# Kernel tuning notes

Hardware: AMD Instinct MI355X
Metric: run time of the kernel (lower is better)

## Reference

```python
import jax, jax.numpy as jnp
import numpy as np

D_MODEL = 1024
HEADS = 16
DK = D_MODEL // HEADS
B, S = 2, 2048


def setup_inputs() -> dict:
    key = jax.random.key(0)
    ks = jax.random.split(key, 9)
    s = 0.02
    return {
        "Q": jax.random.normal(ks[0], (B, S, D_MODEL), jnp.float32),
        "K": jax.random.normal(ks[1], (B, S, D_MODEL), jnp.float32),
        "V": jax.random.normal(ks[2], (B, S, D_MODEL), jnp.float32),
        "mask": jnp.ones((B, 1, S), jnp.int32),
        "Wq": jax.random.normal(ks[3], (D_MODEL, D_MODEL), jnp.float32) * s,
        "Wk": jax.random.normal(ks[4], (D_MODEL, D_MODEL), jnp.float32) * s,
        "Wv": jax.random.normal(ks[5], (D_MODEL, D_MODEL), jnp.float32) * s,
        "Wo": jax.random.normal(ks[6], (D_MODEL, D_MODEL), jnp.float32) * s,
        "ln_gamma": jnp.ones((D_MODEL,), jnp.float32),
        "ln_beta": jnp.zeros((D_MODEL,), jnp.float32),
    }


def _layer_norm(x, gamma, beta, eps=1e-5):
    mu = jnp.mean(x, axis=-1, keepdims=True)
    var = jnp.mean(jnp.square(x - mu), axis=-1, keepdims=True)
    return (x - mu) * jax.lax.rsqrt(var + eps) * gamma + beta


def reference(Q, K, V, mask, Wq, Wk, Wv, Wo, ln_gamma, ln_beta):
    # torch Linear(no bias): y = x @ W.T
    def split_heads(x):  # [B,S,D] -> [B,H,S,dk]
        return x.reshape(B, -1, HEADS, DK).transpose(0, 2, 1, 3)

    q = split_heads(Q @ Wq.T)
    k = split_heads(K @ Wk.T)
    v = split_heads(V @ Wv.T)

    # scores: [B,H,Sq,Sk]
    scores = jnp.einsum("bhqd,bhkd->bhqk", q, k) / np.sqrt(DK).astype(np.float32)
    m = mask[:, None, :, :]  # [B,1,1,S] broadcast over heads and queries
    scores = jnp.where(m == 0, -jnp.inf, scores)
    attn = jax.nn.softmax(scores, axis=-1)  # dropout is identity in eval
    out = jnp.einsum("bhqk,bhkd->bhqd", attn, v)
    out = out.transpose(0, 2, 1, 3).reshape(B, -1, D_MODEL)
    out = out @ Wo.T
    return _layer_norm(out + Q, ln_gamma, ln_beta)
```

## Files before the change

kernel.cpp:

```cpp
#include <hip/hip_runtime.h>
#include <hip/hip_bf16.h>
#include <stdint.h>

#define NB 2
#define NS 2048
#define ND 1024
#define NH 16
#define NDK 64
#define NM (NB*NS)

using bf16x8 = __attribute__((ext_vector_type(8))) short;
using f32x4  = __attribute__((ext_vector_type(4))) float;
using f32x16 = __attribute__((ext_vector_type(16))) float;
using u32x4  = __attribute__((ext_vector_type(4))) unsigned;

__device__ __forceinline__ unsigned short f2bf(float f){
  unsigned u = __float_as_uint(f);
  u += 0x7fffu + ((u>>16)&1u);
  return (unsigned short)(u>>16);
}

__device__ __forceinline__ void gload_lds16(const void* g, void* l){
  __builtin_amdgcn_global_load_lds((const __attribute__((address_space(1))) void*)g,
                                   (__attribute__((address_space(3))) void*)l, 16, 0, 0);
}

__device__ __forceinline__ float fexp2(float x){
#if __has_builtin(__builtin_amdgcn_exp2f)
  return __builtin_amdgcn_exp2f(x);
#else
  return __expf(x * 0.69314718056f);
#endif
}

__device__ __forceinline__ unsigned cvtpk_bf16(float lo, float hi){
  unsigned r;
  asm("v_cvt_pk_bf16_f32 %0, %1, %2" : "=v"(r) : "v"(lo), "v"(hi));
  return r;
}

__device__ __forceinline__ void swap32(unsigned &a, unsigned &b){
#if __has_builtin(__builtin_amdgcn_permlane32_swap)
  auto rr = __builtin_amdgcn_permlane32_swap((int)a, (int)b, false, false);
  a = (unsigned)rr[0]; b = (unsigned)rr[1];
#else
  const bool lo = (threadIdx.x & 32) == 0;
  unsigned sa = (unsigned)__shfl_xor((int)a, 32, 64);
  unsigned sb = (unsigned)__shfl_xor((int)b, 32, 64);
  unsigned na = lo ? a : sb;
  unsigned nb = lo ? sa : b;
  a = na; b = nb;
#endif
}

__device__ __forceinline__ f32x16 mfma32(bf16x8 a, bf16x8 b, f32x16 c){
  return __builtin_amdgcn_mfma_f32_32x32x16_bf16(a, b, c, 0, 0, 0);
}

__global__ __launch_bounds__(256) void prep_k(const float* __restrict__ Q, const float* __restrict__ K,
                                              const float* __restrict__ V, const float* __restrict__ Wq,
                                              const float* __restrict__ Wk, const float* __restrict__ Wv,
                                              const float* __restrict__ Wo,
                                              unsigned short* __restrict__ Xbf,
                                              unsigned short* __restrict__ Wbf){
  const int bid = blockIdx.x;
  const float* src; unsigned short* dst; int i;
  if (bid < 12288){
    const int which = bid >> 12;
    src = (which==0) ? Q : (which==1) ? K : V;
    dst = Xbf + ((size_t)which << 22);
    i = (bid & 4095)*256 + threadIdx.x;
  } else {
    const int which = (bid - 12288) >> 10;
    src = (which==0) ? Wq : (which==1) ? Wk : (which==2) ? Wv : Wo;
    dst = Wbf + ((size_t)which << 20);
    i = ((bid - 12288) & 1023)*256 + threadIdx.x;
  }
  float4 v = ((const float4*)src)[i];
  ushort4 o;
  o.x = f2bf(v.x); o.y = f2bf(v.y); o.z = f2bf(v.z); o.w = f2bf(v.w);
  ((ushort4*)dst)[i] = o;
}

__global__ __launch_bounds__(256) void gemm_qkv(const short* __restrict__ Xbf, const short* __restrict__ Wbf,
                                                unsigned short* __restrict__ qh, unsigned short* __restrict__ kh,
                                                unsigned short* __restrict__ vT){
  __shared__ short lsA[2][4096];
  __shared__ short lsB[2][4096];
  const int tid = threadIdx.x;
  const int hw = blockIdx.x;
  const int logical = (hw & 7)*96 + (hw >> 3);
  const int z = logical >> 8, rem = logical & 255;
  const int my = rem >> 3, nx = rem & 7;
  const short* A = Xbf + (size_t)z*NM*ND;
  const short* W = Wbf + (size_t)z*ND*ND;
  unsigned short* out = (z==0) ? qh : (z==1) ? kh : vT;
  const int mode = (z==2) ? 1 : 0;
  const int m0 = my*128, n0 = nx*128;

  const short* gA = A + (size_t)m0*1024;
  const short* gB = W + (size_t)n0*1024;
  const int srow = tid>>2;
  const int scol = ((tid&3)*8) ^ (((srow>>1)&3)<<3);
  const int w = tid>>6, lane = tid&63, lr = lane&15, lk = lane>>4;
  const int wm = w>>1, wn = w&1;

  f32x4 acc[4][4];
  #pragma unroll
  for (int i=0;i<4;++i)
    #pragma unroll
    for (int j=0;j<4;++j) acc[i][j] = (f32x4){0.f,0.f,0.f,0.f};

  #pragma unroll
  for (int r=0;r<2;++r){
    gload_lds16(gA + (size_t)(r*64+srow)*1024 + scol, &lsA[0][(r*256+tid)*8]);
    gload_lds16(gB + (size_t)(r*64+srow)*1024 + scol, &lsB[0][(r*256+tid)*8]);
  }
  int cur = 0;
  for (int ks=0; ks<32; ++ks){
    __syncthreads();
    if (ks+1 < 32){
      const int k0 = (ks+1)*32;
      #pragma unroll
      for (int r=0;r<2;++r){
        gload_lds16(gA + (size_t)(r*64+srow)*1024 + k0 + scol, &lsA[cur^1][(r*256+tid)*8]);
        gload_lds16(gB + (size_t)(r*64+srow)*1024 + k0 + scol, &lsB[cur^1][(r*256+tid)*8]);
      }
    }
    bf16x8 af[4], bfr[4];
    const char* Ab = (const char*)&lsA[cur][0];
    const char* Bb = (const char*)&lsB[cur][0];
    #pragma unroll
    for (int i=0;i<4;++i){
      const int ra = wm*64 + i*16 + lr;
      const int rb = wn*64 + i*16 + lr;
      af[i]  = *(const bf16x8*)(Ab + ra*64 + ((lk*16) ^ (((ra>>1)&3)<<4)));
      bfr[i] = *(const bf16x8*)(Bb + rb*64 + ((lk*16) ^ (((rb>>1)&3)<<4)));
    }
    #pragma unroll
    for (int i=0;i<4;++i)
      #pragma unroll
      for (int j=0;j<4;++j)
        acc[i][j] = __builtin_amdgcn_mfma_f32_16x16x32_bf16(af[i], bfr[j], acc[i][j], 0,0,0);
    cur ^= 1;
  }
  #pragma unroll
  for (int i=0;i<4;++i)
    #pragma unroll
    for (int j=0;j<4;++j)
      #pragma unroll
      for (int r=0;r<4;++r){
        const int m = m0 + wm*64 + i*16 + lk*4 + r;
        const int n = n0 + wn*64 + j*16 + lr;
        const float v = acc[i][j][r];
        const int b = m>>11, s = m&2047, h = n>>6, dk = n&63;
        size_t addr;
        if (mode == 0) addr = (((size_t)(b*NH+h))*NS + s)*NDK + dk;
        else           addr = (((size_t)(b*NH+h))*NDK + dk)*NS + s;
        out[addr] = f2bf(v);
      }
}

__global__ __launch_bounds__(256) void gemm_out(const short* __restrict__ Attn, const short* __restrict__ Wo,
                                                const float* __restrict__ Qin, float* __restrict__ proj){
  __shared__ short lsA[2][4096];
  __shared__ short lsB[2][4096];
  const int tid = threadIdx.x;
  const int hw = blockIdx.x;
  const int logical = (hw & 7)*32 + (hw >> 3);
  const int my = logical >> 3, nx = logical & 7;
  const int m0 = my*128, n0 = nx*128;
  const short* gA = Attn + (size_t)m0*1024;
  const short* gB = Wo + (size_t)n0*1024;
  const int srow = tid>>2;
  const int scol = ((tid&3)*8) ^ (((srow>>1)&3)<<3);
  const int w = tid>>6, lane = tid&63, lr = lane&15, lk = lane>>4;
  const int wm = w>>1, wn = w&1;

  f32x4 acc[4][4];
  #pragma unroll
  for (int i=0;i<4;++i)
    #pragma unroll
    for (int j=0;j<4;++j) acc[i][j] = (f32x4){0.f,0.f,0.f,0.f};

  #pragma unroll
  for (int r=0;r<2;++r){
    gload_lds16(gA + (size_t)(r*64+srow)*1024 + scol, &lsA[0][(r*256+tid)*8]);
    gload_lds16(gB + (size_t)(r*64+srow)*1024 + scol, &lsB[0][(r*256+tid)*8]);
  }
  int cur = 0;
  for (int ks=0; ks<32; ++ks){
    __syncthreads();
    if (ks+1 < 32){
      const int k0 = (ks+1)*32;
      #pragma unroll
      for (int r=0;r<2;++r){
        gload_lds16(gA + (size_t)(r*64+srow)*1024 + k0 + scol, &lsA[cur^1][(r*256+tid)*8]);
        gload_lds16(gB + (size_t)(r*64+srow)*1024 + k0 + scol, &lsB[cur^1][(r*256+tid)*8]);
      }
    }
    bf16x8 af[4], bfr[4];
    const char* Ab = (const char*)&lsA[cur][0];
    const char* Bb = (const char*)&lsB[cur][0];
    #pragma unroll
    for (int i=0;i<4;++i){
      const int ra = wm*64 + i*16 + lr;
      const int rb = wn*64 + i*16 + lr;
      af[i]  = *(const bf16x8*)(Ab + ra*64 + ((lk*16) ^ (((ra>>1)&3)<<4)));
      bfr[i] = *(const bf16x8*)(Bb + rb*64 + ((lk*16) ^ (((rb>>1)&3)<<4)));
    }
    #pragma unroll
    for (int i=0;i<4;++i)
      #pragma unroll
      for (int j=0;j<4;++j)
        acc[i][j] = __builtin_amdgcn_mfma_f32_16x16x32_bf16(af[i], bfr[j], acc[i][j], 0,0,0);
    cur ^= 1;
  }
  #pragma unroll
  for (int i=0;i<4;++i)
    #pragma unroll
    for (int j=0;j<4;++j)
      #pragma unroll
      for (int r=0;r<4;++r){
        const int m = m0 + wm*64 + i*16 + lk*4 + r;
        const int n = n0 + wn*64 + j*16 + lr;
        proj[(size_t)m*1024 + n] = acc[i][j][r] + Qin[(size_t)m*1024 + n];
      }
}

__global__ __launch_bounds__(512) void attn_k(const short* __restrict__ qh, const short* __restrict__ kh,
                                              const short* __restrict__ vT, const int* __restrict__ mask,
                                              unsigned short* __restrict__ attn){
  __shared__ char sb[65536];
  const int hw = blockIdx.x;
  const int logical = (hw & 7)*64 + (hw >> 3);
  const int qb = logical & 15, h = (logical>>4)&15, b = logical>>8;
  const int tid = threadIdx.x, w = tid>>6, lane = tid&63;
  const int ql = lane & 31, hi = lane>>5;
  const int qw = w & 3, half = w>>2;
  const int bh = b*NH + h;
  const int q0 = qb*128 + qw*32;
  const float C2 = 0.18033688f;

  const int D = tid*16;
  const int strow = D>>7;
  const int S = D ^ ((strow&7)<<4);
  const char* ksrc = (const char*)(kh + (size_t)bh*NS*NDK) + S;
  const char* vsrc = (const char*)(vT + ((size_t)bh*NDK + strow)*NS) + (S & 127);

  const short* qrow = qh + ((size_t)bh*NS + q0 + ql)*NDK + hi*8;
  bf16x8 qf[4];
  #pragma unroll
  for (int kp=0;kp<4;++kp) qf[kp] = *(const bf16x8*)(qrow + kp*16);

  const int* mrow = mask + b*NS + half*1024;

  gload_lds16(ksrc,                      sb + D);
  gload_lds16(ksrc + (size_t)1024*128,   sb + 8192 + D);
  gload_lds16(vsrc,                      sb + 32768 + D);
  gload_lds16(vsrc + (size_t)1024*2,     sb + 32768 + 8192 + D);

  f32x16 o0, o1;
  #pragma unroll
  for (int r=0;r<16;++r){ o0[r]=0.f; o1[r]=0.f; }
  float mrun = -1e30f, lrun = 0.f;

  const int swz = (ql&7)<<4;

  for (int t=0; t<16; ++t){
    const int buf = (t&1)*16384;
    __syncthreads();
    if (t+1 < 16){
      const int nbuf = ((t+1)&1)*16384;
      const size_t kvn0 = (size_t)(t+1)*64, kvn1 = 1024 + kvn0;
      gload_lds16(ksrc + kvn0*128, sb + nbuf + D);
      gload_lds16(ksrc + kvn1*128, sb + nbuf + 8192 + D);
      gload_lds16(vsrc + kvn0*2,   sb + 32768 + nbuf + D);
      gload_lds16(vsrc + kvn1*2,   sb + 32768 + nbuf + 8192 + D);
    }
    const unsigned long long bal = __ballot(mrow[t*64 + lane] != 0);
    const unsigned mw0 = (unsigned)bal, mw1 = (unsigned)(bal>>32);
    const bool allm = (~bal) == 0ull;

    const char* kb = sb + buf + half*8192;
    const char* vb = sb + 32768 + buf + half*8192;

    bf16x8 kf[8];
    #pragma unroll
    for (int kvh=0;kvh<2;++kvh)
      #pragma unroll
      for (int kp=0;kp<4;++kp)
        kf[kvh*4+kp] = *(const bf16x8*)(kb + (((kvh*32+ql)*128 + kp*32 + hi*16) ^ swz));

    f32x16 s0, s1;
    #pragma unroll
    for (int r=0;r<16;++r){ s0[r]=0.f; s1[r]=0.f; }
    __builtin_amdgcn_s_setprio(1);
    #pragma unroll
    for (int kp=0;kp<4;++kp){
      s0 = mfma32(kf[kp],   qf[kp], s0);
      s1 = mfma32(kf[4+kp], qf[kp], s1);
    }
    __builtin_amdgcn_s_setprio(0);

    float t16[16];
    #pragma unroll
    for (int r=0;r<16;++r) t16[r] = fmaxf(s0[r], s1[r]);
    #pragma unroll
    for (int st=8; st>=1; st>>=1)
      #pragma unroll
      for (int r=0;r<st;++r) t16[r] = fmaxf(t16[r], t16[r+st]);
    const float tm = fmaxf(t16[0], __shfl_xor(t16[0], 32, 64));

    if (!__all(tm - mrun <= 32.f)){
      const float mnew = fmaxf(mrun, tm);
      const float fac  = fexp2((mrun - mnew)*C2);
      mrun = mnew;
      #pragma unroll
      for (int r=0;r<16;++r){ o0[r]*=fac; o1[r]*=fac; }
      lrun *= fac;
    }
    const float nb = mrun*C2;

    bf16x8 vf[8];
    #pragma unroll
    for (int dh=0;dh<2;++dh)
      #pragma unroll
      for (int c=0;c<4;++c)
        vf[dh*4+c] = *(const bf16x8*)(vb + (((dh*32+ql)*128 + c*32 + hi*16) ^ swz));

    float psum = 0.f;
    #pragma unroll
    for (int kvh=0; kvh<2; ++kvh){
      const f32x16& ss = kvh ? s1 : s0;
      const unsigned mw = kvh ? mw1 : mw0;
      unsigned pwd[8];
      float ps0 = 0.f, ps1 = 0.f;
      #pragma unroll
      for (int i=0;i<8;++i){
        const int bp0 = ((2*i)&3) + 8*((2*i)>>2);
        float p0 = fexp2(ss[2*i]*C2   - nb);
        float p1 = fexp2(ss[2*i+1]*C2 - nb);
        if (!allm){
          p0 = ((mw >> (bp0     + 4*hi)) & 1u) ? p0 : 0.f;
          p1 = ((mw >> (bp0 + 1 + 4*hi)) & 1u) ? p1 : 0.f;
        }
        ps0 += p0; ps1 += p1;
        pwd[i] = cvtpk_bf16(p0, p1);
      }
      psum += ps0 + ps1;
      swap32(pwd[0], pwd[2]);
      swap32(pwd[1], pwd[3]);
      swap32(pwd[4], pwd[6]);
      swap32(pwd[5], pwd[7]);
      u32x4 c0w = {pwd[0], pwd[1], pwd[2], pwd[3]};
      u32x4 c1w = {pwd[4], pwd[5], pwd[6], pwd[7]};
      bf16x8 pf0 = __builtin_bit_cast(bf16x8, c0w);
      bf16x8 pf1 = __builtin_bit_cast(bf16x8, c1w);
      __builtin_amdgcn_s_setprio(1);
      o0 = mfma32(vf[2*kvh],       pf0, o0);
      o1 = mfma32(vf[4 + 2*kvh],   pf0, o1);
      o0 = mfma32(vf[2*kvh + 1],   pf1, o0);
      o1 = mfma32(vf[4 + 2*kvh+1], pf1, o1);
      __builtin_amdgcn_s_setprio(0);
    }
    psum += __shfl_xor(psum, 32, 64);
    lrun += psum;
  }

  __syncthreads();
  float* smm = (float*)(sb + 32768);
  float* sml = (float*)(sb + 32768 + 1024);
  if (hi == 0){ smm[w*32 + ql] = mrun; sml[w*32 + ql] = lrun; }
  __syncthreads();
  const float pmv = smm[(w^4)*32 + ql], plv = sml[(w^4)*32 + ql];
  const float mfin = fmaxf(mrun, pmv);
  const float facS = fexp2((mrun - mfin)*C2);
  if (w >= 4){
    float* eg = (float*)(sb + (size_t)(w-4)*8192);
    #pragma unroll
    for (int r=0;r<16;++r){
      eg[ql + 32*(hi*16 + r)]        = o0[r]*facS;
      eg[ql + 32*(hi*16 + r) + 1024] = o1[r]*facS;
    }
  }
  __syncthreads();
  if (w < 4){
    float* eg = (float*)(sb + (size_t)w*8192);
    #pragma unroll
    for (int r=0;r<16;++r){
      o0[r] = o0[r]*facS + eg[ql + 32*(hi*16 + r)];
      o1[r] = o1[r]*facS + eg[ql + 32*(hi*16 + r) + 1024];
    }
    const float facP = fexp2((pmv - mfin)*C2);
    const float lfin = lrun*facS + plv*facP;
    const float inv = 1.f / lfin;
    asm volatile("s_waitcnt lgkmcnt(0)" ::: "memory");
    char* ep = sb + (size_t)w*8192;
    #pragma unroll
    for (int dh=0; dh<2; ++dh){
      const f32x16& oo = dh ? o1 : o0;
      #pragma unroll
      for (int i=0;i<8;++i){
        const int d0 = ((2*i)&3) + 8*((2*i)>>2) + 4*hi + dh*32;
        const unsigned pk = cvtpk_bf16(oo[2*i]*inv, oo[2*i+1]*inv);
        *(unsigned*)(ep + (((ql*128) + d0*2) ^ ((ql&7)<<4))) = pk;
      }
    }
    asm volatile("s_waitcnt lgkmcnt(0)" ::: "memory");
    #pragma unroll
    for (int seg=0; seg<4; ++seg){
      const int qq = seg*8 + (lane>>3), dc = (lane&7)*8;
      bf16x8 vv = *(const bf16x8*)(ep + (((qq*128) + dc*2) ^ ((qq&7)<<4)));
      *(bf16x8*)(attn + ((size_t)b*NS + q0 + qq)*ND + h*NDK + dc) = vv;
    }
  }
}

__global__ __launch_bounds__(256) void ln_k(const float* __restrict__ proj,
                                            const float* __restrict__ gamma, const float* __restrict__ beta,
                                            float* __restrict__ out){
  const int row = blockIdx.x*4 + (threadIdx.x>>6);
  const int lane = threadIdx.x & 63;
  const float4* pp = (const float4*)(proj + (size_t)row*ND);
  float4 x[4];
  float sum = 0.f;
  #pragma unroll
  for (int i=0;i<4;++i){
    x[i] = pp[lane + i*64];
    sum += x[i].x + x[i].y + x[i].z + x[i].w;
  }
  #pragma unroll
  for (int off=32; off>=1; off>>=1) sum += __shfl_xor(sum, off, 64);
  const float mu = sum * (1.f/1024.f);
  float vs = 0.f;
  #pragma unroll
  for (int i=0;i<4;++i){
    float d0=x[i].x-mu, d1=x[i].y-mu, d2=x[i].z-mu, d3=x[i].w-mu;
    vs += d0*d0 + d1*d1 + d2*d2 + d3*d3;
  }
  #pragma unroll
  for (int off=32; off>=1; off>>=1) vs += __shfl_xor(vs, off, 64);
  const float rstd = rsqrtf(vs*(1.f/1024.f) + 1e-5f);
  #pragma unroll
  for (int i=0;i<4;++i){
    const float4 g  = ((const float4*)gamma)[lane + i*64];
    const float4 be = ((const float4*)beta)[lane + i*64];
    float4 y;
    y.x = (x[i].x-mu)*rstd*g.x + be.x;
    y.y = (x[i].y-mu)*rstd*g.y + be.y;
    y.z = (x[i].z-mu)*rstd*g.z + be.z;
    y.w = (x[i].w-mu)*rstd*g.w + be.w;
    ((float4*)(out + (size_t)row*ND))[lane + i*64] = y;
  }
}

extern "C" void kernel_launch(void* const* d_in, const int* in_sizes, int n_in,
                              void* d_out, int out_size, void* d_ws, size_t ws_size,
                              hipStream_t stream){
  const float* Q    = (const float*)d_in[0];
  const float* K    = (const float*)d_in[1];
  const float* V    = (const float*)d_in[2];
  const int*   mask = (const int*)  d_in[3];
  const float* Wq   = (const float*)d_in[4];
  const float* Wk   = (const float*)d_in[5];
  const float* Wv   = (const float*)d_in[6];
  const float* Wo   = (const float*)d_in[7];
  const float* gam  = (const float*)d_in[8];
  const float* bet  = (const float*)d_in[9];
  float* out = (float*)d_out;
  char* ws = (char*)d_ws;

  unsigned short* Wbf  = (unsigned short*)(ws);
  unsigned short* Xbf  = (unsigned short*)(ws + (size_t)(8u<<20));
  unsigned short* qhp  = (unsigned short*)(ws + (size_t)(32u<<20));
  unsigned short* khp  = (unsigned short*)(ws + (size_t)(40u<<20));
  unsigned short* vTp  = (unsigned short*)(ws + (size_t)(48u<<20));
  unsigned short* attb = (unsigned short*)(ws + (size_t)(56u<<20));
  float* proj  = (float*)(ws + (size_t)(8u<<20));

  prep_k<<<16384,256,0,stream>>>(Q, K, V, Wq, Wk, Wv, Wo, Xbf, Wbf);

  gemm_qkv<<<768,256,0,stream>>>((const short*)Xbf, (const short*)Wbf, qhp, khp, vTp);

  attn_k<<<512,512,0,stream>>>((const short*)qhp, (const short*)khp, (const short*)vTp, mask, attb);

  gemm_out<<<256,256,0,stream>>>((const short*)attb, (const short*)(Wbf + (3u<<20)), Q, proj);

  ln_k<<<1024,256,0,stream>>>(proj, gam, bet, out);
}
```

Before: 168.9 us.

## Drop split-KV within attention block; each wave processes full key range

The attention kernel previously used 8 waves per block, with two groups each covering half of the key sequence, then merged their partial softmax states through shared memory. It now uses 4 waves per block that each walk all 32 key tiles, which removes the cross-half merge and its extra barriers and halves the LDS footprint. In exchange each wave has a serial loop twice as long, and there are fewer waves per block to hide latency. The smaller LDS footprint may allow more blocks to be resident per CU.

```diff
diff --git a/kernel.cpp b/kernel.cpp
--- a/kernel.cpp
+++ b/kernel.cpp
@@ -228,37 +228,37 @@
       }
 }
 
-__global__ __launch_bounds__(512) void attn_k(const short* __restrict__ qh, const short* __restrict__ kh,
+__global__ __launch_bounds__(256) void attn_k(const short* __restrict__ qh, const short* __restrict__ kh,
                                               const short* __restrict__ vT, const int* __restrict__ mask,
                                               unsigned short* __restrict__ attn){
-  __shared__ char sb[65536];
+  __shared__ char sb[32768];
   const int hw = blockIdx.x;
   const int logical = (hw & 7)*64 + (hw >> 3);
   const int qb = logical & 15, h = (logical>>4)&15, b = logical>>8;
   const int tid = threadIdx.x, w = tid>>6, lane = tid&63;
   const int ql = lane & 31, hi = lane>>5;
-  const int qw = w & 3, half = w>>2;
   const int bh = b*NH + h;
-  const int q0 = qb*128 + qw*32;
+  const int q0 = qb*128 + w*32;
   const float C2 = 0.18033688f;
 
   const int D = tid*16;
   const int strow = D>>7;
-  const int S = D ^ ((strow&7)<<4);
-  const char* ksrc = (const char*)(kh + (size_t)bh*NS*NDK) + S;
-  const char* vsrc = (const char*)(vT + ((size_t)bh*NDK + strow)*NS) + (S & 127);
+  const int scb = (D&127) ^ ((strow&7)<<4);
+  const char* ksrcb = (const char*)kh + (size_t)bh*NS*NDK*2;
+  const char* vsrcb = (const char*)vT + (size_t)bh*NDK*NS*2;
 
   const short* qrow = qh + ((size_t)bh*NS + q0 + ql)*NDK + hi*8;
   bf16x8 qf[4];
   #pragma unroll
   for (int kp=0;kp<4;++kp) qf[kp] = *(const bf16x8*)(qrow + kp*16);
 
-  const int* mrow = mask + b*NS + half*1024;
-
-  gload_lds16(ksrc,                      sb + D);
-  gload_lds16(ksrc + (size_t)1024*128,   sb + 8192 + D);
-  gload_lds16(vsrc,                      sb + 32768 + D);
-  gload_lds16(vsrc + (size_t)1024*2,     sb + 32768 + 8192 + D);
+  const int* mrow = mask + b*NS;
+
+  #pragma unroll
+  for (int p=0;p<2;++p){
+    gload_lds16(ksrcb + (size_t)(p*32+strow)*128 + scb,            sb + p*4096 + D);
+    gload_lds16(vsrcb + (size_t)(p*32+strow)*4096 + scb,           sb + 16384 + p*4096 + D);
+  }
 
   f32x16 o0, o1;
   #pragma unroll
@@ -267,23 +267,25 @@
 
   const int swz = (ql&7)<<4;
 
-  for (int t=0; t<16; ++t){
-    const int buf = (t&1)*16384;
+  for (int t=0; t<32; ++t){
+    const int kv0 = t*64;
+    const int buf = (t&1)*8192;
     __syncthreads();
-    if (t+1 < 16){
-      const int nbuf = ((t+1)&1)*16384;
-      const size_t kvn0 = (size_t)(t+1)*64, kvn1 = 1024 + kvn0;
-      gload_lds16(ksrc + kvn0*128, sb + nbuf + D);
-      gload_lds16(ksrc + kvn1*128, sb + nbuf + 8192 + D);
-      gload_lds16(vsrc + kvn0*2,   sb + 32768 + nbuf + D);
-      gload_lds16(vsrc + kvn1*2,   sb + 32768 + nbuf + 8192 + D);
-    }
-    const unsigned long long bal = __ballot(mrow[t*64 + lane] != 0);
+    if (t+1 < 32){
+      const int nbuf = ((t+1)&1)*8192;
+      const int kvn = kv0 + 64;
+      #pragma unroll
+      for (int p=0;p<2;++p){
+        gload_lds16(ksrcb + (size_t)(kvn + p*32 + strow)*128 + scb,          sb + nbuf + p*4096 + D);
+        gload_lds16(vsrcb + (size_t)(p*32+strow)*4096 + kvn*2 + scb,         sb + 16384 + nbuf + p*4096 + D);
+      }
+    }
+    const unsigned long long bal = __ballot(mrow[kv0 + lane] != 0);
     const unsigned mw0 = (unsigned)bal, mw1 = (unsigned)(bal>>32);
     const bool allm = (~bal) == 0ull;
 
-    const char* kb = sb + buf + half*8192;
-    const char* vb = sb + 32768 + buf + half*8192;
+    const char* kb = sb + buf;
+    const char* vb = sb + 16384 + buf;
 
     bf16x8 kf[8];
     #pragma unroll
@@ -369,51 +371,24 @@
   }
 
   __syncthreads();
-  float* smm = (float*)(sb + 32768);
-  float* sml = (float*)(sb + 32768 + 1024);
-  if (hi == 0){ smm[w*32 + ql] = mrun; sml[w*32 + ql] = lrun; }
-  __syncthreads();
-  const float pmv = smm[(w^4)*32 + ql], plv = sml[(w^4)*32 + ql];
-  const float mfin = fmaxf(mrun, pmv);
-  const float facS = fexp2((mrun - mfin)*C2);
-  if (w >= 4){
-    float* eg = (float*)(sb + (size_t)(w-4)*8192);
-    #pragma unroll
-    for (int r=0;r<16;++r){
-      eg[ql + 32*(hi*16 + r)]        = o0[r]*facS;
-      eg[ql + 32*(hi*16 + r) + 1024] = o1[r]*facS;
-    }
-  }
-  __syncthreads();
-  if (w < 4){
-    float* eg = (float*)(sb + (size_t)w*8192);
-    #pragma unroll
-    for (int r=0;r<16;++r){
-      o0[r] = o0[r]*facS + eg[ql + 32*(hi*16 + r)];
-      o1[r] = o1[r]*facS + eg[ql + 32*(hi*16 + r) + 1024];
-    }
-    const float facP = fexp2((pmv - mfin)*C2);
-    const float lfin = lrun*facS + plv*facP;
-    const float inv = 1.f / lfin;
-    asm volatile("s_waitcnt lgkmcnt(0)" ::: "memory");
-    char* ep = sb + (size_t)w*8192;
-    #pragma unroll
-    for (int dh=0; dh<2; ++dh){
-      const f32x16& oo = dh ? o1 : o0;
-      #pragma unroll
-      for (int i=0;i<8;++i){
-        const int d0 = ((2*i)&3) + 8*((2*i)>>2) + 4*hi + dh*32;
-        const unsigned pk = cvtpk_bf16(oo[2*i]*inv, oo[2*i+1]*inv);
-        *(unsigned*)(ep + (((ql*128) + d0*2) ^ ((ql&7)<<4))) = pk;
-      }
-    }
-    asm volatile("s_waitcnt lgkmcnt(0)" ::: "memory");
-    #pragma unroll
-    for (int seg=0; seg<4; ++seg){
-      const int qq = seg*8 + (lane>>3), dc = (lane&7)*8;
-      bf16x8 vv = *(const bf16x8*)(ep + (((qq*128) + dc*2) ^ ((qq&7)<<4)));
-      *(bf16x8*)(attn + ((size_t)b*NS + q0 + qq)*ND + h*NDK + dc) = vv;
-    }
+  const float inv = 1.f / lrun;
+  char* ep = sb + w*4096;
+  #pragma unroll
+  for (int dh=0; dh<2; ++dh){
+    const f32x16& oo = dh ? o1 : o0;
+    #pragma unroll
+    for (int i=0;i<8;++i){
+      const int d0 = ((2*i)&3) + 8*((2*i)>>2) + 4*hi + dh*32;
+      const unsigned pk = cvtpk_bf16(oo[2*i]*inv, oo[2*i+1]*inv);
+      *(unsigned*)(ep + (((ql*128) + d0*2) ^ ((ql&7)<<4))) = pk;
+    }
+  }
+  asm volatile("s_waitcnt lgkmcnt(0)" ::: "memory");
+  #pragma unroll
+  for (int seg=0; seg<4; ++seg){
+    const int qq = seg*8 + (lane>>3), dc = (lane&7)*8;
+    bf16x8 vv = *(const bf16x8*)(ep + (((qq*128) + dc*2) ^ ((qq&7)<<4)));
+    *(bf16x8*)(attn + ((size_t)b*NS + q0 + qq)*ND + h*NDK + dc) = vv;
   }
 }
 
@@ -483,7 +458,7 @@
 
   gemm_qkv<<<768,256,0,stream>>>((const short*)Xbf, (const short*)Wbf, qhp, khp, vTp);
 
-  attn_k<<<512,512,0,stream>>>((const short*)qhp, (const short*)khp, (const short*)vTp, mask, attb);
+  attn_k<<<512,256,0,stream>>>((const short*)qhp, (const short*)khp, (const short*)vTp, mask, attb);
 
   gemm_out<<<256,256,0,stream>>>((const short*)attb, (const short*)(Wbf + (3u<<20)), Q, proj);
 
```

After: 164.4 us. 2.6% less time.
